# Performance work log

Measured on AMD Instinct MI355X. Metric: run time of the kernel, lower is better.

## Reference

```python
import jax, jax.numpy as jnp
import numpy as np

HIDDEN = 32
DN = ('NCHW', 'OIHW', 'NCHW')


def setup_inputs() -> dict:
    key = jax.random.key(0)
    ks = jax.random.split(key, 16)
    B = 32768
    s = lambda *sh: 1.0 / np.sqrt(np.prod(sh[1:]) if len(sh) > 1 else sh[0])
    inp = {
        'x': jax.random.normal(ks[0], (B, 12, 3, 4, 4), jnp.float32),
        'hour': jax.random.uniform(ks[1], (B, 1), jnp.float32),
        # ConvLSTM cell: Conv2d(3+32 -> 4*32, k=3, pad=1)
        'conv_w': jax.random.normal(ks[2], (4 * HIDDEN, 3 + HIDDEN, 3, 3), jnp.float32) * 0.05,
        'conv_b': jnp.zeros((4 * HIDDEN,), jnp.float32),
        # hour embedding: Linear(1,16) -> ReLU -> Linear(16,32)
        'he_w1': jax.random.normal(ks[3], (1, 16), jnp.float32),
        'he_b1': jnp.zeros((16,), jnp.float32),
        'he_w2': jax.random.normal(ks[4], (16, 32), jnp.float32) * 0.25,
        'he_b2': jnp.zeros((32,), jnp.float32),
        # decoder: Linear(544,256) -> ReLU -> Linear(256,128) -> ReLU -> Linear(128,30) -> Sigmoid
        'd_w1': jax.random.normal(ks[5], (32 * 4 * 4 + 32, 256), jnp.float32) * 0.04,
        'd_b1': jnp.zeros((256,), jnp.float32),
        'd_w2': jax.random.normal(ks[6], (256, 128), jnp.float32) * 0.06,
        'd_b2': jnp.zeros((128,), jnp.float32),
        'd_w3': jax.random.normal(ks[7], (128, 30), jnp.float32) * 0.09,
        'd_b3': jnp.zeros((30,), jnp.float32),
    }
    return inp


def _convlstm_scan(x, conv_w, conv_b):
    B, T, C, H, W = x.shape
    h0 = jnp.zeros((B, HIDDEN, H, W), x.dtype)
    c0 = jnp.zeros((B, HIDDEN, H, W), x.dtype)

    def step(carry, xt):
        h, c = carry
        inp = jnp.concatenate([xt, h], axis=1)  # [B, 3+32, 4, 4]
        gates = jax.lax.conv_general_dilated(
            inp, conv_w, (1, 1), 'SAME', dimension_numbers=DN)
        gates = gates + conv_b[None, :, None, None]
        i, f, o, g = jnp.split(gates, 4, axis=1)
        c_next = jax.nn.sigmoid(f) * c + jax.nn.sigmoid(i) * jnp.tanh(g)
        h_next = jax.nn.sigmoid(o) * jnp.tanh(c_next)
        return (h_next, c_next), None

    xs = jnp.swapaxes(x, 0, 1)  # [T, B, C, H, W]
    (h, c), _ = jax.lax.scan(step, (h0, c0), xs)
    return h


def reference(x, hour, conv_w, conv_b, he_w1, he_b1, he_w2, he_b2,
              d_w1, d_b1, d_w2, d_b2, d_w3, d_b3):
    B = x.shape[0]
    h = _convlstm_scan(x, conv_w, conv_b)            # [B, 32, 4, 4]
    spatial = h.reshape(B, -1)                        # [B, 512]
    hf = jax.nn.relu(hour @ he_w1 + he_b1) @ he_w2 + he_b2  # [B, 32]
    z = jnp.concatenate([spatial, hf], axis=1)        # [B, 544]
    z = jax.nn.relu(z @ d_w1 + d_b1)
    z = jax.nn.relu(z @ d_w2 + d_b2)                  # (dropout is identity in eval)
    out = jax.nn.sigmoid(z @ d_w3 + d_b3)
    return out.reshape(B, 10, 3)
```

## Files before the change

kernel.cpp:

```cpp
#include <hip/hip_runtime.h>

typedef _Float16 f16;
typedef _Float16 f16x4 __attribute__((ext_vector_type(4)));
typedef _Float16 f16x8 __attribute__((ext_vector_type(8)));
typedef float f32x2 __attribute__((ext_vector_type(2)));
typedef float f32x4 __attribute__((ext_vector_type(4)));

#define MFMA16(a, b, c) __builtin_amdgcn_mfma_f32_16x16x32_f16((a), (b), (c), 0, 0, 0)

__device__ __forceinline__ float rcp_(float x) { return __builtin_amdgcn_rcpf(x); }
__device__ __forceinline__ float sigm(float v) { return rcp_(1.0f + __expf(-v)); }
__device__ __forceinline__ float tanh_(float v) { return 1.0f - 2.0f * rcp_(__expf(2.0f * v) + 1.0f); }
__device__ __forceinline__ float exp2_(float x) { return __builtin_amdgcn_exp2f(x); }

#define LOG2E 1.4426950408889634f
#define HCELL 80
#define HSAMP 2880
#define HBUFB 11520
#define XP0 23040
#define XBUFB 1152
#define AR 25344
#define WSO 25344
#define SMEMA 50688
#define NGRP 8192
#define GRID_REC 512

extern "C" __global__ __launch_bounds__(256, 2)
void hwq_rec(const float* __restrict__ gx, const float* __restrict__ ghour,
             const float* __restrict__ gcw, const float* __restrict__ gcb,
             const float* __restrict__ ghw1, const float* __restrict__ ghb1,
             const float* __restrict__ ghw2, const float* __restrict__ ghb2,
             f16* __restrict__ wz)
{
  __shared__ __align__(16) char smem[SMEMA];
  const int tid = threadIdx.x;
  const int lane = tid & 63;
  const int wv = tid >> 6;
  const int mg = wv & 1;
  const int ng = wv >> 1;
  const int lr = lane & 15;
  const int lk = lane >> 4;
  const int TOFF[9] = {0, 1, 2, 6, 7, 8, 12, 13, 14};
  const int pp0 = (lr >> 2) * 6 + (lr & 3);

  f16x8 Ax1[4], Ax2[4];
  {
    f16* axs = (f16*)(smem + WSO);
    for (int i = tid; i < 4096; i += 256) {
      int m = i >> 5, k = i & 31;
      int tau = k >> 2, sl = k & 3;
      int oc = ((m & 3) << 5) + (m >> 2);
      float sc = ((m & 3) == 3) ? (2.0f * LOG2E) : (-LOG2E);
      f16 v = (f16)0.0f;
      if (sl < 3) v = (f16)(sc * gcw[oc * 315 + sl * 9 + tau]);
      else if (tau == 4) v = (f16)(sc * gcb[oc]);
      axs[i] = v;
    }
    __syncthreads();
    #pragma unroll
    for (int mt = 0; mt < 4; ++mt) {
      Ax1[mt] = *(const f16x8*)(smem + WSO + (mg * 64 + mt * 16 + lr) * 64 + lk * 16);
      int m = mg * 64 + mt * 16 + lr;
      int oc = ((m & 3) << 5) + (m >> 2);
      float sc = ((m & 3) == 3) ? (2.0f * LOG2E) : (-LOG2E);
      f16x8 f = {(f16)0, (f16)0, (f16)0, (f16)0, (f16)0, (f16)0, (f16)0, (f16)0};
      if (lk == 0) {
        f[0] = (f16)(sc * gcw[oc * 315 + 8]);
        f[1] = (f16)(sc * gcw[oc * 315 + 17]);
        f[2] = (f16)(sc * gcw[oc * 315 + 26]);
      }
      Ax2[mt] = f;
    }
    __syncthreads();
  }
  f16x8 Ah[9][4];
  {
    f16* wst = (f16*)(smem + WSO);
    #pragma unroll
    for (int c = 0; c < 4; ++c) {
      for (int i = tid; i < 9216; i += 256) {
        int mrow = i / 288, rem = i - mrow * 288;
        int m = c * 32 + mrow;
        int oc = ((m & 3) << 5) + (m >> 2);
        float sc = ((m & 3) == 3) ? (2.0f * LOG2E) : (-LOG2E);
        wst[i] = (f16)(sc * gcw[oc * 315 + 27 + rem]);
      }
      __syncthreads();
      if (mg == (c >> 1)) {
        #pragma unroll
        for (int mtl = 0; mtl < 2; ++mtl) {
          int mt = (c & 1) * 2 + mtl;
          #pragma unroll
          for (int tap = 0; tap < 9; ++tap) {
            f16x8 f;
            #pragma unroll
            for (int j = 0; j < 8; ++j)
              f[j] = wst[(mtl * 16 + lr) * 288 + (lk * 8 + j) * 9 + tap];
            Ah[tap][mt] = f;
          }
        }
      }
      __syncthreads();
    }
  }
  {
    float* za = (float*)smem;
    for (int i = tid; i < 12672; i += 256) za[i] = 0.0f;
    __syncthreads();
    {
      int ar = tid >> 7, xb = (tid >> 6) & 1, b = (tid >> 4) & 3, p = tid & 15;
      int cell = ((p >> 2) + 1) * 6 + (p & 3) + 1;
      *(f16*)(smem + ar * AR + XP0 + xb * XBUFB + b * 288 + cell * 8 + 6) = (f16)1.0f;
    }
    __syncthreads();
  }

  const int hb  = (ng * 2) * HSAMP + pp0 * HCELL + lk * 16;
  const int xpb = XP0 + (ng * 2) * 288 + pp0 * 8;
  const int wb  = (ng * 2) * HSAMP + (pp0 + 7) * HCELL + (mg * 16 + lk) * 2;
  const int xo0 = TOFF[2 * lk] * 8;
  const int xo1 = TOFF[2 * lk + 1] * 8;
  const bool stg = tid < 192;
  const int sb = tid / 48, srem = tid - sb * 48;
  const int sp = srem & 15, sic = srem >> 4;
  const int xdst = XP0 + sb * 288 + (((sp >> 2) + 1) * 6 + (sp & 3) + 1) * 8 + sic * 2;
  const int zb_ = tid >> 6, zc16 = (tid >> 2) & 15, zpart = tid & 3;
  const int zaddr = zb_ * HSAMP + ((zc16 >> 2) * 6 + (zc16 & 3) + 7) * HCELL + zpart * 16;

  const f32x4 Z0v = {0.f, 0.f, 0.f, 0.f};

#define XPH(ab, nt) { \
    const int base_ = (ab) + xrb + xpb + (nt) * 288; \
    f16x4 lo_ = *(const f16x4*)(smem + base_ + xo0); \
    f16x4 hi_ = *(const f16x4*)(smem + base_ + xo1); \
    f16x8 bf1_ = __builtin_shufflevector(lo_, hi_, 0, 1, 2, 3, 4, 5, 6, 7); \
    f16x4 l8_ = *(const f16x4*)(smem + base_ + 112); \
    f16x8 bf2_ = __builtin_shufflevector(l8_, l8_, 0, 1, 2, 3, 0, 1, 2, 3); \
    _Pragma("unroll") for (int mt = 0; mt < 4; ++mt) { \
      acc[mt][nt] = MFMA16(Ax1[mt], bf1_, Z0v); \
      acc[mt][nt] = MFMA16(Ax2[mt], bf2_, acc[mt][nt]); } }

#define TAPS(ab, nt) \
    _Pragma("unroll") for (int tap = 0; tap < 9; ++tap) { \
      f16x8 bf_ = *(const f16x8*)(smem + (ab) + rb + hb + TOFF[tap] * HCELL + (nt) * HSAMP); \
      _Pragma("unroll") for (int mt = 0; mt < 4; ++mt) \
        acc[mt][nt] = MFMA16(Ah[tap][mt], bf_, acc[mt][nt]); }

#define UPD_L(g, ab, mt, nt) { \
    float Ei = exp2_(acc[mt][nt][0]); \
    float Ef = exp2_(acc[mt][nt][1]); \
    float Eo = exp2_(acc[mt][nt][2]); \
    float Eg = exp2_(acc[mt][nt][3]); \
    float fg = rcp_(1.0f + Ef); \
    float pq = rcp_((1.0f + Ei) * (1.0f + Eg)); \
    float cn = fmaf(fg, cst[g][mt][nt], (2.0f * LOG2E) * ((Eg - 1.0f) * pq)); \
    cst[g][mt][nt] = cn; \
    float Ec = exp2_(cn); \
    *(f16*)(smem + (ab) + wbuf + wb + (nt) * HSAMP + (mt) * 8) = \
        (f16)((Ec - 1.0f) * rcp_((1.0f + Eo) * (1.0f + Ec))); }

#define UPD_G(g, bgv, mt, nt) { \
    float Ei = exp2_(acc[mt][nt][0]); \
    float Ef = exp2_(acc[mt][nt][1]); \
    float Eo = exp2_(acc[mt][nt][2]); \
    float Eg = exp2_(acc[mt][nt][3]); \
    float fg = rcp_(1.0f + Ef); \
    float pq = rcp_((1.0f + Ei) * (1.0f + Eg)); \
    float cn = fmaf(fg, cst[g][mt][nt], (2.0f * LOG2E) * ((Eg - 1.0f) * pq)); \
    float Ec = exp2_(cn); \
    wz[(size_t)((bgv) + ng * 2 + (nt)) * 544 + (mg * 16 + (mt) * 4 + lk) * 16 + lr] = \
        (f16)((Ec - 1.0f) * rcp_((1.0f + Eo) * (1.0f + Ec))); }

  for (int it = 0; it < 8; ++it) {
    const int gA = blockIdx.x + (2 * it) * GRID_REC;
    const int gB = gA + GRID_REC;
    const int bgA = gA << 2, bgB = gB << 2;
    const float* xsrcA = gx + (size_t)bgA * 576 + (size_t)sb * 576 + srem;
    const float* xsrcB = gx + (size_t)bgB * 576 + (size_t)sb * 576 + srem;

    {
      f32x2 z2 = {0.f, 0.f};
      *(f32x2*)(smem + zaddr) = z2;
      *(f32x2*)(smem + zaddr + 8) = z2;
      *(f32x2*)(smem + AR + zaddr) = z2;
      *(f32x2*)(smem + AR + zaddr + 8) = z2;
    }
    if (stg) {
      *(f16*)(smem + xdst) = (f16)xsrcA[0];
      *(f16*)(smem + AR + xdst) = (f16)xsrcB[0];
    }
    float cst[2][4][2];
    #pragma unroll
    for (int g = 0; g < 2; ++g)
      #pragma unroll
      for (int mt = 0; mt < 4; ++mt) { cst[g][mt][0] = 0.0f; cst[g][mt][1] = 0.0f; }
    __syncthreads();

    for (int t = 0; t < 11; ++t) {
      const int rb   = (t & 1) * HBUFB;
      const int xrb  = (t & 1) * XBUFB;
      const int wbuf = HBUFB - rb;
      float xvA = 0.0f, xvB = 0.0f;
      if (stg) { xvA = xsrcA[(t + 1) * 48]; xvB = xsrcB[(t + 1) * 48]; }

      f32x4 acc[4][2];
      XPH(0, 0); TAPS(0, 0);
      XPH(0, 1); TAPS(0, 1);
      UPD_L(0, 0, 0, 0); UPD_L(0, 0, 1, 0); UPD_L(0, 0, 2, 0); UPD_L(0, 0, 3, 0);
      XPH(AR, 0); TAPS(AR, 0);
      UPD_L(0, 0, 0, 1); UPD_L(0, 0, 1, 1); UPD_L(0, 0, 2, 1); UPD_L(0, 0, 3, 1);
      XPH(AR, 1); TAPS(AR, 1);
      UPD_L(1, AR, 0, 0); UPD_L(1, AR, 1, 0); UPD_L(1, AR, 2, 0); UPD_L(1, AR, 3, 0);
      UPD_L(1, AR, 0, 1); UPD_L(1, AR, 1, 1); UPD_L(1, AR, 2, 1); UPD_L(1, AR, 3, 1);

      if (stg) {
        *(f16*)(smem + (XBUFB - xrb) + xdst) = (f16)xvA;
        *(f16*)(smem + AR + (XBUFB - xrb) + xdst) = (f16)xvB;
      }
      __syncthreads();
    }

    {
      const int rb  = HBUFB;
      const int xrb = XBUFB;
      f32x4 acc[4][2];
      XPH(0, 0); TAPS(0, 0);
      XPH(0, 1); TAPS(0, 1);
      UPD_G(0, bgA, 0, 0); UPD_G(0, bgA, 1, 0); UPD_G(0, bgA, 2, 0); UPD_G(0, bgA, 3, 0);
      XPH(AR, 0); TAPS(AR, 0);
      UPD_G(0, bgA, 0, 1); UPD_G(0, bgA, 1, 1); UPD_G(0, bgA, 2, 1); UPD_G(0, bgA, 3, 1);
      XPH(AR, 1); TAPS(AR, 1);
      UPD_G(1, bgB, 0, 0); UPD_G(1, bgB, 1, 0); UPD_G(1, bgB, 2, 0); UPD_G(1, bgB, 3, 0);
      UPD_G(1, bgB, 0, 1); UPD_G(1, bgB, 1, 1); UPD_G(1, bgB, 2, 1); UPD_G(1, bgB, 3, 1);

      {
        int b = tid >> 5, k2 = tid & 31;
        int smp = (b < 4) ? (bgA + b) : (bgB + b - 4);
        float h0 = ghour[smp];
        float a = ghb2[k2];
        #pragma unroll
        for (int ii = 0; ii < 16; ++ii) {
          float u = fmaxf(h0 * ghw1[ii] + ghb1[ii], 0.0f);
          a += u * ghw2[ii * 32 + k2];
        }
        wz[(size_t)smp * 544 + 512 + k2] = (f16)a;
      }
    }
  }
#undef XPH
#undef TAPS
#undef UPD_L
#undef UPD_G
}

extern "C" __global__ void hwq_prep(const float* __restrict__ gdw1,
                                    const float* __restrict__ gdw2,
                                    const float* __restrict__ gdw3,
                                    f16* __restrict__ w1t, f16* __restrict__ w2t,
                                    f16* __restrict__ w3t)
{
  int i0 = blockIdx.x * 256 + threadIdx.x;
  int stride = gridDim.x * 256;
  for (int idx = i0; idx < 139264; idx += stride) {
    int n = idx / 544, k = idx - n * 544;
    w1t[idx] = (f16)gdw1[k * 256 + n];
  }
  for (int idx = i0; idx < 32768; idx += stride) {
    int n = idx >> 8, k = idx & 255;
    w2t[idx] = (f16)gdw2[k * 128 + n];
  }
  for (int idx = i0; idx < 4096; idx += stride) {
    int n = idx >> 7, k = idx & 127;
    w3t[idx] = (n < 30) ? (f16)gdw3[k * 30 + n] : (f16)0.0f;
  }
}

extern "C" __global__ __launch_bounds__(256, 2)
void hwq_dec(const f16* __restrict__ wz, const f16* __restrict__ w1t,
             const f16* __restrict__ w2t, const f16* __restrict__ w3t,
             const float* __restrict__ gdb1, const float* __restrict__ gdb2,
             const float* __restrict__ gdb3, float* __restrict__ gout)
{
  __shared__ __align__(16) char smem[55296];
  f16* a1 = (f16*)smem;
  f16* a2 = (f16*)(smem + 35840);
  const int tid = threadIdx.x;
  const int lane = tid & 63;
  const int wv = tid >> 6;
  const int lr = lane & 15;
  const int lk = lane >> 4;
  const int s0 = blockIdx.x << 6;

  f32x4 acc1[4][4];
  #pragma unroll
  for (int nt = 0; nt < 4; ++nt) {
    float bb = gdb1[wv * 64 + nt * 16 + lr];
    f32x4 bv = {bb, bb, bb, bb};
    #pragma unroll
    for (int mt = 0; mt < 4; ++mt) acc1[mt][nt] = bv;
  }
  for (int kt = 0; kt < 17; ++kt) {
    f16x8 af[4];
    #pragma unroll
    for (int mt = 0; mt < 4; ++mt)
      af[mt] = *(const f16x8*)(wz + (size_t)(s0 + mt * 16 + lr) * 544 + kt * 32 + lk * 8);
    #pragma unroll
    for (int nt = 0; nt < 4; ++nt) {
      f16x8 bf = *(const f16x8*)(w1t + (size_t)(wv * 64 + nt * 16 + lr) * 544 + kt * 32 + lk * 8);
      #pragma unroll
      for (int mt = 0; mt < 4; ++mt)
        acc1[mt][nt] = MFMA16(af[mt], bf, acc1[mt][nt]);
    }
  }
  #pragma unroll
  for (int mt = 0; mt < 4; ++mt)
    #pragma unroll
    for (int nt = 0; nt < 4; ++nt) {
      int n = wv * 64 + nt * 16 + lr;
      #pragma unroll
      for (int r = 0; r < 4; ++r)
        a1[(mt * 16 + lk * 4 + r) * 280 + n] = (f16)fmaxf(acc1[mt][nt][r], 0.0f);
    }
  __syncthreads();

  f32x4 acc2[4][2];
  #pragma unroll
  for (int nt = 0; nt < 2; ++nt) {
    float bb = gdb2[wv * 32 + nt * 16 + lr];
    f32x4 bv = {bb, bb, bb, bb};
    #pragma unroll
    for (int mt = 0; mt < 4; ++mt) acc2[mt][nt] = bv;
  }
  for (int kt = 0; kt < 8; ++kt) {
    f16x8 af[4];
    #pragma unroll
    for (int mt = 0; mt < 4; ++mt)
      af[mt] = *(const f16x8*)(a1 + (mt * 16 + lr) * 280 + kt * 32 + lk * 8);
    #pragma unroll
    for (int nt = 0; nt < 2; ++nt) {
      f16x8 bf = *(const f16x8*)(w2t + (size_t)(wv * 32 + nt * 16 + lr) * 256 + kt * 32 + lk * 8);
      #pragma unroll
      for (int mt = 0; mt < 4; ++mt)
        acc2[mt][nt] = MFMA16(af[mt], bf, acc2[mt][nt]);
    }
  }
  __syncthreads();
  #pragma unroll
  for (int mt = 0; mt < 4; ++mt)
    #pragma unroll
    for (int nt = 0; nt < 2; ++nt) {
      int n = wv * 32 + nt * 16 + lr;
      #pragma unroll
      for (int r = 0; r < 4; ++r)
        a2[(mt * 16 + lk * 4 + r) * 152 + n] = (f16)fmaxf(acc2[mt][nt][r], 0.0f);
    }
  __syncthreads();

  if (wv < 2) {
    int n = wv * 16 + lr;
    float bb = (n < 30) ? gdb3[n] : 0.0f;
    f32x4 acc3[4];
    #pragma unroll
    for (int mt = 0; mt < 4; ++mt) { f32x4 bv = {bb, bb, bb, bb}; acc3[mt] = bv; }
    #pragma unroll
    for (int kt = 0; kt < 4; ++kt) {
      f16x8 bf = *(const f16x8*)(w3t + n * 128 + kt * 32 + lk * 8);
      #pragma unroll
      for (int mt = 0; mt < 4; ++mt) {
        f16x8 af = *(const f16x8*)(a2 + (mt * 16 + lr) * 152 + kt * 32 + lk * 8);
        acc3[mt] = MFMA16(af, bf, acc3[mt]);
      }
    }
    if (n < 30) {
      #pragma unroll
      for (int mt = 0; mt < 4; ++mt)
        #pragma unroll
        for (int r = 0; r < 4; ++r)
          gout[(size_t)(s0 + mt * 16 + lk * 4 + r) * 30 + n] = sigm(acc3[mt][r]);
    }
  }
}

typedef _Float16 f16x4m __attribute__((ext_vector_type(4)));
#define OFF_B 46080
#define SMEM_BYTES (46080 + 17408)

extern "C" __global__ __launch_bounds__(256, 1)
void hwq_fused_mono(const float* __restrict__ gx, const float* __restrict__ ghour,
               const float* __restrict__ gcw, const float* __restrict__ gcb,
               const float* __restrict__ ghw1, const float* __restrict__ ghb1,
               const float* __restrict__ ghw2, const float* __restrict__ ghb2,
               const float* __restrict__ gdw1, const float* __restrict__ gdb1,
               const float* __restrict__ gdw2, const float* __restrict__ gdb2,
               const float* __restrict__ gdw3, const float* __restrict__ gdb3,
               float* __restrict__ gout)
{
  __shared__ __align__(16) char smem[SMEM_BYTES];
  const int tid = threadIdx.x;
  const int lane = tid & 63;
  const int wv = tid >> 6;
  const int mg = wv & 1;
  const int ng = wv >> 1;
  const int lr = lane & 15;
  const int lk = lane >> 4;
  const int bg = blockIdx.x << 4;

  f16x8 Ah[9][4];
  {
    f16* wst = (f16*)(smem);
    #pragma unroll
    for (int c = 0; c < 2; ++c) {
      __syncthreads();
      for (int i = tid; i < 18432; i += 256) {
        int oc = i / 288, rem = i - oc * 288;
        wst[i] = (f16)gcw[(c * 64 + oc) * 315 + 27 + rem];
      }
      __syncthreads();
      #pragma unroll
      for (int g = 0; g < 2; ++g) {
        int ocl = g * 32 + mg * 16 + lr;
        #pragma unroll
        for (int tap = 0; tap < 9; ++tap) {
          f16x8 f;
          #pragma unroll
          for (int j = 0; j < 8; ++j)
            f[j] = wst[ocl * 288 + (lk * 8 + j) * 9 + tap];
          Ah[tap][c * 2 + g] = f;
        }
      }
    }
  }
  f16x8 Ax[4];
  {
    f16* xw = (f16*)(smem + OFF_B);
    __syncthreads();
    for (int i = tid; i < 3456; i += 256) {
      int oc = i / 27, rem = i - oc * 27;
      xw[i] = (f16)gcw[oc * 315 + rem];
    }
    __syncthreads();
    #pragma unroll
    for (int mt = 0; mt < 4; ++mt) {
      int oc = mt * 32 + mg * 16 + lr;
      f16x8 f;
      #pragma unroll
      for (int j = 0; j < 8; ++j) {
        int k = lk * 8 + j;
        int tap = (k * 11) >> 5;
        int ic = k - 3 * tap;
        f16 v = (f16)0.0f;
        if (k < 27) v = xw[oc * 27 + ic * 9 + tap];
        f[j] = v;
      }
      Ax[mt] = f;
    }
    __syncthreads();
  }

  float bias[4][4];
  #pragma unroll
  for (int mt = 0; mt < 4; ++mt)
    #pragma unroll
    for (int r = 0; r < 4; ++r)
      bias[mt][r] = gcb[mt * 32 + mg * 16 + lk * 4 + r];

  {
    float* za = (float*)smem;
    for (int i = tid; i < 11520; i += 256) za[i] = 0.0f;
    float* zb = (float*)(smem + OFF_B);
    for (int i = tid; i < 1152; i += 256) zb[i] = 0.0f;
    __syncthreads();
    for (int i = tid; i < 768; i += 256) {
      int b = i / 48, rem = i - b * 48;
      int pos = rem & 15;
      int ic = rem >> 4;
      int pp = (pos >> 2) * 6 + (pos & 3) + 7;
      *(f16*)(smem + OFF_B + b * 288 + pp * 8 + ic * 2) =
          (f16)gx[(size_t)(bg + b) * 576 + rem];
    }
    __syncthreads();
  }

  int hbase[8], xbase[8], wbase[8];
  #pragma unroll
  for (int nt = 0; nt < 8; ++nt) {
    int n = ng * 128 + nt * 16 + lr;
    int b = n >> 4, pos = n & 15;
    int pp0 = (pos >> 2) * 6 + (pos & 3);
    hbase[nt] = b * 2880 + pp0 * 80 + lk * 16;
    xbase[nt] = OFF_B + b * 288 + pp0 * 8;
    wbase[nt] = b * 2880 + (pp0 + 7) * 80 + (mg * 16 + lk * 4) * 2;
  }
  int xoff[8], xval[8];
  #pragma unroll
  for (int j = 0; j < 8; ++j) {
    int k = lk * 8 + j;
    int tap = (k * 11) >> 5;
    int ic = k - 3 * tap;
    xoff[j] = ((tap / 3) * 6 + (tap % 3)) * 8 + ic * 2;
    xval[j] = (k < 27);
  }

  const int TOFF[9] = {0, 1, 2, 6, 7, 8, 12, 13, 14};

  f32x4 cst[8];
  #pragma unroll
  for (int nt = 0; nt < 8; ++nt) { f32x4 z = {0.f, 0.f, 0.f, 0.f}; cst[nt] = z; }

  for (int t = 0; t < 12; ++t) {
    f32x4 acc[4][8];
    #pragma unroll
    for (int mt = 0; mt < 4; ++mt) {
      f32x4 bi = {bias[mt][0], bias[mt][1], bias[mt][2], bias[mt][3]};
      #pragma unroll
      for (int nt = 0; nt < 8; ++nt) acc[mt][nt] = bi;
    }
    #pragma unroll
    for (int tap = 0; tap < 9; ++tap) {
      #pragma unroll
      for (int nt = 0; nt < 8; ++nt) {
        f16x8 bf = *(const f16x8*)(smem + hbase[nt] + TOFF[tap] * 80);
        #pragma unroll
        for (int mt = 0; mt < 4; ++mt)
          acc[mt][nt] = MFMA16(Ah[tap][mt], bf, acc[mt][nt]);
      }
    }
    #pragma unroll
    for (int nt = 0; nt < 8; ++nt) {
      f16x8 bf;
      #pragma unroll
      for (int j = 0; j < 8; ++j) {
        int a = xval[j] ? (xbase[nt] + xoff[j]) : OFF_B;
        bf[j] = *(const f16*)(smem + a);
      }
      #pragma unroll
      for (int mt = 0; mt < 4; ++mt)
        acc[mt][nt] = MFMA16(Ax[mt], bf, acc[mt][nt]);
    }
    __syncthreads();

    #pragma unroll
    for (int nt = 0; nt < 8; ++nt) {
      f16 hh[4];
      #pragma unroll
      for (int r = 0; r < 4; ++r) {
        float ig = sigm(acc[0][nt][r]);
        float fg = sigm(acc[1][nt][r]);
        float og = sigm(acc[2][nt][r]);
        float gg = tanh_(acc[3][nt][r]);
        float cn = fg * cst[nt][r] + ig * gg;
        cst[nt][r] = cn;
        hh[r] = (f16)(og * tanh_(cn));
      }
      if (t < 11) {
        f16x4m hv = {hh[0], hh[1], hh[2], hh[3]};
        *(f16x4m*)(smem + wbase[nt]) = hv;
      } else {
        int n = ng * 128 + nt * 16 + lr;
        int b = n >> 4, pos = n & 15;
        int ch0 = mg * 16 + lk * 4;
        #pragma unroll
        for (int r = 0; r < 4; ++r)
          *(f16*)(smem + OFF_B + b * 1088 + (ch0 + r) * 32 + pos * 2) = hh[r];
      }
    }
    if (t < 11) {
      for (int i = tid; i < 768; i += 256) {
        int b = i / 48, rem = i - b * 48;
        int pos = rem & 15;
        int ic = rem >> 4;
        int pp = (pos >> 2) * 6 + (pos & 3) + 7;
        *(f16*)(smem + OFF_B + b * 288 + pp * 8 + ic * 2) =
            (f16)gx[(size_t)(bg + b) * 576 + (t + 1) * 48 + rem];
      }
    } else {
      for (int i = tid; i < 512; i += 256) {
        int b = i >> 5, k2 = i & 31;
        float h0 = ghour[bg + b];
        float a = ghb2[k2];
        #pragma unroll
        for (int ii = 0; ii < 16; ++ii) {
          float u = fmaxf(h0 * ghw1[ii] + ghb1[ii], 0.0f);
          a += u * ghw2[ii * 32 + k2];
        }
        *(f16*)(smem + OFF_B + b * 1088 + (512 + k2) * 2) = (f16)a;
      }
    }
    __syncthreads();
  }

  f16* zz  = (f16*)(smem + OFF_B);
  f16* wch = (f16*)(smem);
  f16* a1  = (f16*)(smem + 16384);
  f16* a2  = (f16*)(smem + 24576);
  f16* w3s = (f16*)(smem + 28672);

  f32x4 acc1[4];
  #pragma unroll
  for (int i = 0; i < 4; ++i) { f32x4 z = {0.f, 0.f, 0.f, 0.f}; acc1[i] = z; }
  for (int kt = 0; kt < 17; ++kt) {
    __syncthreads();
    for (int i = tid; i < 8192; i += 256) {
      int k = i >> 8, n = i & 255;
      wch[i] = (f16)gdw1[(kt * 32 + k) * 256 + n];
    }
    __syncthreads();
    f16x8 af = *(const f16x8*)((char*)zz + lr * 1088 + (kt * 32 + lk * 8) * 2);
    #pragma unroll
    for (int nt = 0; nt < 4; ++nt) {
      int n = (wv * 4 + nt) * 16 + lr;
      f16x8 bf;
      #pragma unroll
      for (int j = 0; j < 8; ++j) bf[j] = wch[(lk * 8 + j) * 256 + n];
      acc1[nt] = MFMA16(af, bf, acc1[nt]);
    }
  }
  __syncthreads();
  #pragma unroll
  for (int nt = 0; nt < 4; ++nt) {
    int n = (wv * 4 + nt) * 16 + lr;
    float bb = gdb1[n];
    #pragma unroll
    for (int r = 0; r < 4; ++r)
      a1[(lk * 4 + r) * 256 + n] = (f16)fmaxf(acc1[nt][r] + bb, 0.0f);
  }

  f32x4 acc2[2];
  #pragma unroll
  for (int i = 0; i < 2; ++i) { f32x4 z = {0.f, 0.f, 0.f, 0.f}; acc2[i] = z; }
  for (int kt = 0; kt < 8; ++kt) {
    __syncthreads();
    for (int i = tid; i < 4096; i += 256) {
      int k = i >> 7, n = i & 127;
      wch[i] = (f16)gdw2[(kt * 32 + k) * 128 + n];
    }
    __syncthreads();
    f16x8 af = *(const f16x8*)((char*)a1 + lr * 512 + (kt * 32 + lk * 8) * 2);
    #pragma unroll
    for (int nt = 0; nt < 2; ++nt) {
      int n = (wv * 2 + nt) * 16 + lr;
      f16x8 bf;
      #pragma unroll
      for (int j = 0; j < 8; ++j) bf[j] = wch[(lk * 8 + j) * 128 + n];
      acc2[nt] = MFMA16(af, bf, acc2[nt]);
    }
  }
  __syncthreads();
  #pragma unroll
  for (int nt = 0; nt < 2; ++nt) {
    int n = (wv * 2 + nt) * 16 + lr;
    float bb = gdb2[n];
    #pragma unroll
    for (int r = 0; r < 4; ++r)
      a2[(lk * 4 + r) * 128 + n] = (f16)fmaxf(acc2[nt][r] + bb, 0.0f);
  }
  __syncthreads();

  for (int i = tid; i < 4096; i += 256) {
    int k = i >> 5, n = i & 31;
    w3s[i] = (n < 30) ? (f16)gdw3[k * 30 + n] : (f16)0.0f;
  }
  __syncthreads();
  if (wv < 2) {
    f32x4 acc3 = {0.f, 0.f, 0.f, 0.f};
    int n = wv * 16 + lr;
    #pragma unroll
    for (int kt = 0; kt < 4; ++kt) {
      f16x8 af = *(const f16x8*)((char*)a2 + lr * 256 + (kt * 32 + lk * 8) * 2);
      f16x8 bf;
      #pragma unroll
      for (int j = 0; j < 8; ++j) bf[j] = w3s[(kt * 32 + lk * 8 + j) * 32 + n];
      acc3 = MFMA16(af, bf, acc3);
    }
    if (n < 30) {
      float bb = gdb3[n];
      #pragma unroll
      for (int r = 0; r < 4; ++r) {
        float v = sigm(acc3[r] + bb);
        gout[(size_t)(bg + lk * 4 + r) * 30 + n] = v;
      }
    }
  }
}

extern "C" void kernel_launch(void* const* d_in, const int* in_sizes, int n_in,
                              void* d_out, int out_size, void* d_ws, size_t ws_size,
                              hipStream_t stream) {
  (void)in_sizes; (void)n_in; (void)out_size;
  const size_t W1OFF = 35651584;
  const size_t W2OFF = W1OFF + 278528;
  const size_t W3OFF = W2OFF + 65536;
  const size_t NEED  = W3OFF + 8192;
  if (ws_size >= NEED) {
    f16* wzp = (f16*)d_ws;
    f16* w1t = (f16*)((char*)d_ws + W1OFF);
    f16* w2t = (f16*)((char*)d_ws + W2OFF);
    f16* w3t = (f16*)((char*)d_ws + W3OFF);
    hwq_prep<<<256, 256, 0, stream>>>((const float*)d_in[8], (const float*)d_in[10],
                                      (const float*)d_in[12], w1t, w2t, w3t);
    hwq_rec<<<GRID_REC, 256, 0, stream>>>(
        (const float*)d_in[0], (const float*)d_in[1], (const float*)d_in[2],
        (const float*)d_in[3], (const float*)d_in[4], (const float*)d_in[5],
        (const float*)d_in[6], (const float*)d_in[7], wzp);
    hwq_dec<<<512, 256, 0, stream>>>(wzp, w1t, w2t, w3t,
                                     (const float*)d_in[9], (const float*)d_in[11],
                                     (const float*)d_in[13], (float*)d_out);
  } else {
    hwq_fused_mono<<<2048, 256, 0, stream>>>(
        (const float*)d_in[0],  (const float*)d_in[1],  (const float*)d_in[2],
        (const float*)d_in[3],  (const float*)d_in[4],  (const float*)d_in[5],
        (const float*)d_in[6],  (const float*)d_in[7],  (const float*)d_in[8],
        (const float*)d_in[9],  (const float*)d_in[10], (const float*)d_in[11],
        (const float*)d_in[12], (const float*)d_in[13], (float*)d_out);
  }
}
```

Measured before the change: 643.3 us.

## Interleave three sample groups per recurrence step instead of two

The recurrent ConvLSTM kernel now processes three independent 4-sample groups at once, interleaving their MFMA tap work and gate updates. This gives more independent work to hide latency between the serial timestep barriers. A final single-group tail pass covers the 16th group per block, since 16 is not divisible by 3. Shared memory grows from about 50KB to 76KB per block, which may reduce occupancy below the two-blocks-per-CU launch bound, and register pressure rises because of the extra cell state.

```diff
diff --git a/kernel.cpp b/kernel.cpp
--- a/kernel.cpp
+++ b/kernel.cpp
@@ -21,8 +21,7 @@
 #define XBUFB 1152
 #define AR 25344
 #define WSO 25344
-#define SMEMA 50688
-#define NGRP 8192
+#define SMEMA 76032
 #define GRID_REC 512
 
 extern "C" __global__ __launch_bounds__(256, 2)
@@ -105,10 +104,10 @@
   }
   {
     float* za = (float*)smem;
-    for (int i = tid; i < 12672; i += 256) za[i] = 0.0f;
-    __syncthreads();
-    {
-      int ar = tid >> 7, xb = (tid >> 6) & 1, b = (tid >> 4) & 3, p = tid & 15;
+    for (int i = tid; i < 19008; i += 256) za[i] = 0.0f;
+    __syncthreads();
+    for (int i = tid; i < 384; i += 256) {
+      int ar = i >> 7, xb = (i >> 6) & 1, b = (i >> 4) & 3, p = i & 15;
       int cell = ((p >> 2) + 1) * 6 + (p & 3) + 1;
       *(f16*)(smem + ar * AR + XP0 + xb * XBUFB + b * 288 + cell * 8 + 6) = (f16)1.0f;
     }
@@ -171,27 +170,31 @@
     wz[(size_t)((bgv) + ng * 2 + (nt)) * 544 + (mg * 16 + (mt) * 4 + lk) * 16 + lr] = \
         (f16)((Ec - 1.0f) * rcp_((1.0f + Eo) * (1.0f + Ec))); }
 
-  for (int it = 0; it < 8; ++it) {
-    const int gA = blockIdx.x + (2 * it) * GRID_REC;
-    const int gB = gA + GRID_REC;
-    const int bgA = gA << 2, bgB = gB << 2;
-    const float* xsrcA = gx + (size_t)bgA * 576 + (size_t)sb * 576 + srem;
-    const float* xsrcB = gx + (size_t)bgB * 576 + (size_t)sb * 576 + srem;
+  const int base_g = blockIdx.x << 4;
+
+  for (int ti = 0; ti < 5; ++ti) {
+    const int g0 = base_g + ti * 3;
+    const int bg0 = g0 << 2;
+    const float* xs0 = gx + (size_t)(bg0 + sb) * 576 + srem;
+    const float* xs1 = xs0 + 4 * 576;
+    const float* xs2 = xs0 + 8 * 576;
 
     {
       f32x2 z2 = {0.f, 0.f};
-      *(f32x2*)(smem + zaddr) = z2;
-      *(f32x2*)(smem + zaddr + 8) = z2;
-      *(f32x2*)(smem + AR + zaddr) = z2;
-      *(f32x2*)(smem + AR + zaddr + 8) = z2;
+      #pragma unroll
+      for (int a = 0; a < 3; ++a) {
+        *(f32x2*)(smem + a * AR + zaddr) = z2;
+        *(f32x2*)(smem + a * AR + zaddr + 8) = z2;
+      }
     }
     if (stg) {
-      *(f16*)(smem + xdst) = (f16)xsrcA[0];
-      *(f16*)(smem + AR + xdst) = (f16)xsrcB[0];
-    }
-    float cst[2][4][2];
-    #pragma unroll
-    for (int g = 0; g < 2; ++g)
+      *(f16*)(smem + xdst) = (f16)xs0[0];
+      *(f16*)(smem + AR + xdst) = (f16)xs1[0];
+      *(f16*)(smem + 2 * AR + xdst) = (f16)xs2[0];
+    }
+    float cst[3][4][2];
+    #pragma unroll
+    for (int g = 0; g < 3; ++g)
       #pragma unroll
       for (int mt = 0; mt < 4; ++mt) { cst[g][mt][0] = 0.0f; cst[g][mt][1] = 0.0f; }
     __syncthreads();
@@ -200,8 +203,8 @@
       const int rb   = (t & 1) * HBUFB;
       const int xrb  = (t & 1) * XBUFB;
       const int wbuf = HBUFB - rb;
-      float xvA = 0.0f, xvB = 0.0f;
-      if (stg) { xvA = xsrcA[(t + 1) * 48]; xvB = xsrcB[(t + 1) * 48]; }
+      float xv0 = 0.0f, xv1 = 0.0f, xv2 = 0.0f;
+      if (stg) { xv0 = xs0[(t + 1) * 48]; xv1 = xs1[(t + 1) * 48]; xv2 = xs2[(t + 1) * 48]; }
 
       f32x4 acc[4][2];
       XPH(0, 0); TAPS(0, 0);
@@ -211,11 +214,16 @@
       UPD_L(0, 0, 0, 1); UPD_L(0, 0, 1, 1); UPD_L(0, 0, 2, 1); UPD_L(0, 0, 3, 1);
       XPH(AR, 1); TAPS(AR, 1);
       UPD_L(1, AR, 0, 0); UPD_L(1, AR, 1, 0); UPD_L(1, AR, 2, 0); UPD_L(1, AR, 3, 0);
+      XPH(2 * AR, 0); TAPS(2 * AR, 0);
       UPD_L(1, AR, 0, 1); UPD_L(1, AR, 1, 1); UPD_L(1, AR, 2, 1); UPD_L(1, AR, 3, 1);
+      XPH(2 * AR, 1); TAPS(2 * AR, 1);
+      UPD_L(2, 2 * AR, 0, 0); UPD_L(2, 2 * AR, 1, 0); UPD_L(2, 2 * AR, 2, 0); UPD_L(2, 2 * AR, 3, 0);
+      UPD_L(2, 2 * AR, 0, 1); UPD_L(2, 2 * AR, 1, 1); UPD_L(2, 2 * AR, 2, 1); UPD_L(2, 2 * AR, 3, 1);
 
       if (stg) {
-        *(f16*)(smem + (XBUFB - xrb) + xdst) = (f16)xvA;
-        *(f16*)(smem + AR + (XBUFB - xrb) + xdst) = (f16)xvB;
+        *(f16*)(smem + (XBUFB - xrb) + xdst) = (f16)xv0;
+        *(f16*)(smem + AR + (XBUFB - xrb) + xdst) = (f16)xv1;
+        *(f16*)(smem + 2 * AR + (XBUFB - xrb) + xdst) = (f16)xv2;
       }
       __syncthreads();
     }
@@ -226,16 +234,20 @@
       f32x4 acc[4][2];
       XPH(0, 0); TAPS(0, 0);
       XPH(0, 1); TAPS(0, 1);
-      UPD_G(0, bgA, 0, 0); UPD_G(0, bgA, 1, 0); UPD_G(0, bgA, 2, 0); UPD_G(0, bgA, 3, 0);
+      UPD_G(0, bg0, 0, 0); UPD_G(0, bg0, 1, 0); UPD_G(0, bg0, 2, 0); UPD_G(0, bg0, 3, 0);
       XPH(AR, 0); TAPS(AR, 0);
-      UPD_G(0, bgA, 0, 1); UPD_G(0, bgA, 1, 1); UPD_G(0, bgA, 2, 1); UPD_G(0, bgA, 3, 1);
+      UPD_G(0, bg0, 0, 1); UPD_G(0, bg0, 1, 1); UPD_G(0, bg0, 2, 1); UPD_G(0, bg0, 3, 1);
       XPH(AR, 1); TAPS(AR, 1);
-      UPD_G(1, bgB, 0, 0); UPD_G(1, bgB, 1, 0); UPD_G(1, bgB, 2, 0); UPD_G(1, bgB, 3, 0);
-      UPD_G(1, bgB, 0, 1); UPD_G(1, bgB, 1, 1); UPD_G(1, bgB, 2, 1); UPD_G(1, bgB, 3, 1);
-
-      {
-        int b = tid >> 5, k2 = tid & 31;
-        int smp = (b < 4) ? (bgA + b) : (bgB + b - 4);
+      UPD_G(1, bg0 + 4, 0, 0); UPD_G(1, bg0 + 4, 1, 0); UPD_G(1, bg0 + 4, 2, 0); UPD_G(1, bg0 + 4, 3, 0);
+      XPH(2 * AR, 0); TAPS(2 * AR, 0);
+      UPD_G(1, bg0 + 4, 0, 1); UPD_G(1, bg0 + 4, 1, 1); UPD_G(1, bg0 + 4, 2, 1); UPD_G(1, bg0 + 4, 3, 1);
+      XPH(2 * AR, 1); TAPS(2 * AR, 1);
+      UPD_G(2, bg0 + 8, 0, 0); UPD_G(2, bg0 + 8, 1, 0); UPD_G(2, bg0 + 8, 2, 0); UPD_G(2, bg0 + 8, 3, 0);
+      UPD_G(2, bg0 + 8, 0, 1); UPD_G(2, bg0 + 8, 1, 1); UPD_G(2, bg0 + 8, 2, 1); UPD_G(2, bg0 + 8, 3, 1);
+
+      for (int i = tid; i < 384; i += 256) {
+        int b = i >> 5, k2 = i & 31;
+        int smp = bg0 + b;
         float h0 = ghour[smp];
         float a = ghb2[k2];
         #pragma unroll
@@ -244,6 +256,60 @@
           a += u * ghw2[ii * 32 + k2];
         }
         wz[(size_t)smp * 544 + 512 + k2] = (f16)a;
+      }
+    }
+  }
+
+  {
+    const int g = base_g + 15;
+    const int bg = g << 2;
+    const float* xs0 = gx + (size_t)(bg + sb) * 576 + srem;
+
+    {
+      f32x2 z2 = {0.f, 0.f};
+      *(f32x2*)(smem + zaddr) = z2;
+      *(f32x2*)(smem + zaddr + 8) = z2;
+    }
+    if (stg) *(f16*)(smem + xdst) = (f16)xs0[0];
+    float cst[1][4][2];
+    #pragma unroll
+    for (int mt = 0; mt < 4; ++mt) { cst[0][mt][0] = 0.0f; cst[0][mt][1] = 0.0f; }
+    __syncthreads();
+
+    for (int t = 0; t < 11; ++t) {
+      const int rb   = (t & 1) * HBUFB;
+      const int xrb  = (t & 1) * XBUFB;
+      const int wbuf = HBUFB - rb;
+      float xv0 = 0.0f;
+      if (stg) xv0 = xs0[(t + 1) * 48];
+
+      f32x4 acc[4][2];
+      XPH(0, 0); TAPS(0, 0);
+      XPH(0, 1); TAPS(0, 1);
+      UPD_L(0, 0, 0, 0); UPD_L(0, 0, 1, 0); UPD_L(0, 0, 2, 0); UPD_L(0, 0, 3, 0);
+      UPD_L(0, 0, 0, 1); UPD_L(0, 0, 1, 1); UPD_L(0, 0, 2, 1); UPD_L(0, 0, 3, 1);
+      if (stg) *(f16*)(smem + (XBUFB - xrb) + xdst) = (f16)xv0;
+      __syncthreads();
+    }
+    {
+      const int rb  = HBUFB;
+      const int xrb = XBUFB;
+      f32x4 acc[4][2];
+      XPH(0, 0); TAPS(0, 0);
+      XPH(0, 1); TAPS(0, 1);
+      UPD_G(0, bg, 0, 0); UPD_G(0, bg, 1, 0); UPD_G(0, bg, 2, 0); UPD_G(0, bg, 3, 0);
+      UPD_G(0, bg, 0, 1); UPD_G(0, bg, 1, 1); UPD_G(0, bg, 2, 1); UPD_G(0, bg, 3, 1);
+
+      if (tid < 128) {
+        int b = tid >> 5, k2 = tid & 31;
+        float h0 = ghour[bg + b];
+        float a = ghb2[k2];
+        #pragma unroll
+        for (int ii = 0; ii < 16; ++ii) {
+          float u = fmaxf(h0 * ghw1[ii] + ghb1[ii], 0.0f);
+          a += u * ghw2[ii * 32 + k2];
+        }
+        wz[(size_t)(bg + b) * 544 + 512 + k2] = (f16)a;
       }
     }
   }
```

After: 1.390 ms. 2.16x slower.
